# Performance work log

Measured on AMD Instinct MI355X. Metric: run time of the kernel, lower is better.

Reference implementation:

```python
import jax, jax.numpy as jnp
import numpy as np

DIM = 1024
HEADS = 16
HEAD_DIM = DIM // HEADS
NEG = -1e30
EPS = 1e-5


def _linear(x, w, b):
    # torch nn.Linear: y = x @ W^T + b, W: [out, in]
    return jnp.einsum('bnd,od->bno', x, w) + b


def _mha(x, ctx, wq, bq, wk, bk, wv, bv, wo, bo, mask):
    B, N, D = x.shape
    M = ctx.shape[1]
    q = _linear(x, wq, bq).reshape(B, N, HEADS, HEAD_DIM).transpose(0, 2, 1, 3)
    k = _linear(ctx, wk, bk).reshape(B, M, HEADS, HEAD_DIM).transpose(0, 2, 1, 3)
    v = _linear(ctx, wv, bv).reshape(B, M, HEADS, HEAD_DIM).transpose(0, 2, 1, 3)
    scores = jnp.einsum('bhqd,bhkd->bhqk', q, k) / np.sqrt(HEAD_DIM).astype(np.float32)
    if mask is not None:
        scores = jnp.where(mask == 0, NEG, scores)
    attn = jax.nn.softmax(scores, axis=-1)  # dropout = identity (eval mode)
    out = jnp.einsum('bhqk,bhkd->bhqd', attn, v)
    out = out.transpose(0, 2, 1, 3).reshape(B, N, D)
    return _linear(out, wo, bo)


def _ln(x, g, b):
    mu = jnp.mean(x, axis=-1, keepdims=True)
    var = jnp.mean(jnp.square(x - mu), axis=-1, keepdims=True)
    return (x - mu) * jax.lax.rsqrt(var + EPS) * g + b


def setup_inputs() -> dict:
    key = jax.random.key(0)
    ks = jax.random.split(key, 24)
    B, N, M = 2, 2048, 1024
    s = 0.02
    d = {
        'x': jax.random.normal(ks[0], (B, N, DIM), jnp.float32),
        'memory': jax.random.normal(ks[1], (B, M, DIM), jnp.float32),
        'mask': jnp.tril(jnp.ones((N, N), jnp.int32))[None, None],
    }
    i = 2
    for p in ['sa', 'ca']:
        for nm in ['q', 'k', 'v', 'o']:
            d[f'{p}_w{nm}'] = jax.random.normal(ks[i], (DIM, DIM), jnp.float32) * s; i += 1
            d[f'{p}_b{nm}'] = jnp.zeros((DIM,), jnp.float32)
    d['ff_w1'] = jax.random.normal(ks[i], (4 * DIM, DIM), jnp.float32) * s; i += 1
    d['ff_b1'] = jnp.zeros((4 * DIM,), jnp.float32)
    d['ff_w2'] = jax.random.normal(ks[i], (DIM, 4 * DIM), jnp.float32) * s; i += 1
    d['ff_b2'] = jnp.zeros((DIM,), jnp.float32)
    for j in (1, 2, 3):
        d[f'ln{j}_g'] = jnp.ones((DIM,), jnp.float32)
        d[f'ln{j}_b'] = jnp.zeros((DIM,), jnp.float32)
    return d


def reference(x, memory, mask,
              sa_wq, sa_bq, sa_wk, sa_bk, sa_wv, sa_bv, sa_wo, sa_bo,
              ca_wq, ca_bq, ca_wk, ca_bk, ca_wv, ca_bv, ca_wo, ca_bo,
              ff_w1, ff_b1, ff_w2, ff_b2,
              ln1_g, ln1_b, ln2_g, ln2_b, ln3_g, ln3_b):
    x = _ln(x + _mha(x, x, sa_wq, sa_bq, sa_wk, sa_bk, sa_wv, sa_bv, sa_wo, sa_bo, mask), ln1_g, ln1_b)
    x = _ln(x + _mha(x, memory, ca_wq, ca_bq, ca_wk, ca_bk, ca_wv, ca_bv, ca_wo, ca_bo, None), ln2_g, ln2_b)
    h = jax.nn.relu(_linear(x, ff_w1, ff_b1))  # dropout = identity (eval)
    x = _ln(x + _linear(h, ff_w2, ff_b2), ln3_g, ln3_b)
    return x
```

## Files before the change

kernel.cpp:

```cpp
#include <hip/hip_runtime.h>


typedef __attribute__((ext_vector_type(8))) short bf16x8;
typedef __attribute__((ext_vector_type(4))) float f32x4;

__device__ __forceinline__ unsigned short f2bf(float f) {
    union { float f; unsigned int u; } v; v.f = f;
    unsigned int r = v.u + 0x7fffu + ((v.u >> 16) & 1u);
    return (unsigned short)(r >> 16);
}
__device__ __forceinline__ float bf2f(unsigned short u) {
    union { unsigned int u; float f; } v; v.u = (unsigned int)u << 16;
    return v.f;
}
__device__ __forceinline__ unsigned int bftrunc(float f) {
    union { float f; unsigned int u; } v; v.f = f;
    return v.u >> 16;
}

struct ConvArgs {
    const float* src[12];
    unsigned short* dst[12];
    int blk_ofs[13];
    int n4[12];
    const float* bq; const float* bk; const float* bv;
    const float* ck; const float* cv;
    float* bqkv; float* bkvc;
};
__global__ __launch_bounds__(256) void conv_multi(ConvArgs a)
{
    int bid = blockIdx.x;
    if (bid >= a.blk_ofs[12]) {
        int i = (bid - a.blk_ofs[12]) * 256 + threadIdx.x;
        if (i < 1024)       a.bqkv[i] = a.bq[i];
        else if (i < 2048)  a.bqkv[i] = a.bk[i - 1024];
        else if (i < 3072)  a.bqkv[i] = a.bv[i - 2048];
        else if (i < 4096)  a.bkvc[i - 3072] = a.ck[i - 3072];
        else if (i < 5120)  a.bkvc[i - 3072] = a.cv[i - 4096];
        return;
    }
    int s = 0;
#pragma unroll
    for (int t = 0; t < 12; ++t) if (bid >= a.blk_ofs[t + 1]) s = t + 1;
    int i = (bid - a.blk_ofs[s]) * 256 + threadIdx.x;
    if (i >= a.n4[s]) return;
    float4 v = ((const float4*)a.src[s])[i];
    ushort4 o;
    o.x = f2bf(v.x); o.y = f2bf(v.y); o.z = f2bf(v.z); o.w = f2bf(v.w);
    ((ushort4*)a.dst[s])[i] = o;
}

template<int TM, int TN, int EPI, int SK>
__device__ __forceinline__ void gemm_body(
    unsigned short (*As)[64], unsigned short (*Bs)[64],
    const unsigned short* __restrict__ A, const unsigned short* __restrict__ W,
    const float* __restrict__ bias, unsigned short* __restrict__ out,
    int K, int Ncols, long slice_stride, int bid, int gx, int zslice)
{
    constexpr int AI = TM / 32;
    constexpr int BJ = TN / 32;

    const int tid  = threadIdx.x;
    const int lane = tid & 63;
    const int wave = tid >> 6;
    const int qd   = lane >> 4;
    const int l15  = lane & 15;
    const int wm   = (wave >> 1) * (TM / 2);
    const int wn   = (wave & 1) * (TN / 2);

    const int gpg = 8 * gx;
    const long m0 = (long)((bid / gpg) * 8 + (bid & 7)) * TM;
    const long n0 = (long)((bid % gpg) >> 3) * TN;

    f32x4 acc[AI][BJ] = {};

    const int srow = lane >> 3;
    const int scol = (((lane & 7) ^ srow)) * 8;
    const unsigned short* Ag = A + (m0 + wave * (8 * AI) + srow) * (long)K + scol;
    const unsigned short* Wg = W + (n0 + wave * (8 * BJ) + srow) * (long)K + scol;

    const int ksl   = K / SK;
    const int kbase = (SK > 1) ? zslice * ksl : 0;

    for (int k0 = kbase; k0 < kbase + ksl; k0 += 64) {
#pragma unroll
        for (int c = 0; c < AI; ++c)
            __builtin_amdgcn_global_load_lds(
                (const __attribute__((address_space(1))) unsigned int*)(Ag + (long)c * 8 * K + k0),
                (__attribute__((address_space(3))) unsigned int*)((char*)&As[0][0] + (wave * AI + c) * 1024),
                16, 0, 0);
#pragma unroll
        for (int c = 0; c < BJ; ++c)
            __builtin_amdgcn_global_load_lds(
                (const __attribute__((address_space(1))) unsigned int*)(Wg + (long)c * 8 * K + k0),
                (__attribute__((address_space(3))) unsigned int*)((char*)&Bs[0][0] + (wave * BJ + c) * 1024),
                16, 0, 0);
        __syncthreads();
#pragma unroll
        for (int kk = 0; kk < 64; kk += 32) {
            const int pg = ((((kk >> 3) + qd)) ^ (l15 & 7)) * 8;
            bf16x8 af[AI], bw[BJ];
#pragma unroll
            for (int i = 0; i < AI; ++i)
                af[i] = *(const bf16x8*)&As[wm + i * 16 + l15][pg];
#pragma unroll
            for (int j = 0; j < BJ; ++j)
                bw[j] = *(const bf16x8*)&Bs[wn + j * 16 + l15][pg];
#pragma unroll
            for (int i = 0; i < AI; ++i)
#pragma unroll
                for (int j = 0; j < BJ; ++j)
                    acc[i][j] = __builtin_amdgcn_mfma_f32_16x16x32_bf16(
                        af[i], bw[j], acc[i][j], 0, 0, 0);
        }
        __syncthreads();
    }

    unsigned short* op = out + ((SK > 1) ? (long)zslice * slice_stride : 0);
#pragma unroll
    for (int j = 0; j < BJ; ++j) {
        long col = n0 + wn + j * 16 + l15;
        float bv = (SK == 1 || zslice == 0) ? bias[col] : 0.f;
#pragma unroll
        for (int i = 0; i < AI; ++i) {
#pragma unroll
            for (int r = 0; r < 4; ++r) {
                long row = m0 + wm + i * 16 + qd * 4 + r;
                float v = acc[i][j][r] + bv;
                if (EPI == 1) v = (v > 0.f) ? v : 0.f;
                op[row * Ncols + col] = f2bf(v);
            }
        }
    }
}

template<int TM, int TN, int EPI, int SK>
__global__ __launch_bounds__(256) void gemm_bt(
    const unsigned short* __restrict__ A, const unsigned short* __restrict__ W,
    const float* __restrict__ bias, unsigned short* __restrict__ out,
    int K, int Ncols, long slice_stride)
{
    __shared__ unsigned short As[TM][64];
    __shared__ unsigned short Bs[TN][64];
    const int bid = blockIdx.y * gridDim.x + blockIdx.x;
    gemm_body<TM, TN, EPI, SK>(As, Bs, A, W, bias, out, K, Ncols, slice_stride,
                               bid, gridDim.x, (int)blockIdx.z);
}

template<int EPI, int SK>
__device__ __forceinline__ void gemm8_body(
    unsigned short* Ab, unsigned short* Bb,
    const unsigned short* __restrict__ A, const unsigned short* __restrict__ W,
    const float* __restrict__ bias, unsigned short* __restrict__ out,
    int K, int Ncols, long slice_stride, int mb, int nb, int zslice)
{
    const int tid  = threadIdx.x;
    const int lane = tid & 63;
    const int wave = tid >> 6;
    const int qd   = lane >> 4;
    const int l15  = lane & 15;
    const int wm   = (wave >> 2) * 128;
    const int wn   = (wave & 3) * 64;

    const long m0 = (long)mb * 256;
    const long n0 = (long)nb * 256;

    const int ksl   = K / SK;
    const int kbase = (SK > 1) ? zslice * ksl : 0;
    const int NG    = ksl / 64;

    f32x4 acc[8][4] = {};

    const int srow = tid >> 3;
    const int sgrp = ((tid & 7) ^ (srow & 7)) * 8;
    const unsigned short* Ag = A + (m0 + srow) * (long)K + kbase + sgrp;
    const unsigned short* Wg = W + (n0 + srow) * (long)K + kbase + sgrp;

    auto stA = [&](int db, int r0, int kt) {
        __builtin_amdgcn_global_load_lds(
            (const __attribute__((address_space(1))) unsigned int*)(Ag + (long)r0 * K + kt * 64),
            (__attribute__((address_space(3))) unsigned int*)(Ab + db * 16384 + r0 * 64 + wave * 512),
            16, 0, 0);
    };
    auto stB = [&](int db, int r0, int kt) {
        __builtin_amdgcn_global_load_lds(
            (const __attribute__((address_space(1))) unsigned int*)(Wg + (long)r0 * K + kt * 64),
            (__attribute__((address_space(3))) unsigned int*)(Bb + db * 16384 + r0 * 64 + wave * 512),
            16, 0, 0);
    };
    auto rdA = [&](int db, int row, int kk) -> bf16x8 {
        const int p = (((kk << 2) + qd) ^ (l15 & 7)) << 3;
        return *(const bf16x8*)(Ab + db * 16384 + row * 64 + p);
    };
    auto rdB = [&](int db, int row, int kk) -> bf16x8 {
        const int p = (((kk << 2) + qd) ^ (l15 & 7)) << 3;
        return *(const bf16x8*)(Bb + db * 16384 + row * 64 + p);
    };

#pragma unroll
    for (int h = 0; h < 4; ++h) stA(0, h * 64, 0);
#pragma unroll
    for (int h = 0; h < 4; ++h) stB(0, h * 64, 0);
    if (NG > 1) {
#pragma unroll
        for (int h = 0; h < 4; ++h) stB(1, h * 64, 1);
        stA(1, 0, 1); stA(1, 128, 1);
        asm volatile("s_waitcnt vmcnt(6)" ::: "memory");
    } else {
        asm volatile("s_waitcnt vmcnt(0)" ::: "memory");
    }
    __builtin_amdgcn_s_barrier();

    for (int g = 0; g < NG; ++g) {
        const int db = g & 1, ob = db ^ 1;
        bf16x8 af[4][2], bw[4][2];

        if (g + 1 < NG) { stA(ob, 64, g + 1); stA(ob, 192, g + 1); }

#pragma unroll
        for (int i = 0; i < 4; ++i)
#pragma unroll
            for (int kk = 0; kk < 2; ++kk)
                af[i][kk] = rdA(db, wm + i * 16 + l15, kk);
#pragma unroll
        for (int j = 0; j < 4; ++j)
#pragma unroll
            for (int kk = 0; kk < 2; ++kk)
                bw[j][kk] = rdB(db, wn + j * 16 + l15, kk);
        __builtin_amdgcn_s_setprio(1);
#pragma unroll
        for (int i = 0; i < 4; ++i)
#pragma unroll
            for (int j = 0; j < 4; ++j) {
                acc[i][j] = __builtin_amdgcn_mfma_f32_16x16x32_bf16(af[i][0], bw[j][0], acc[i][j], 0, 0, 0);
                acc[i][j] = __builtin_amdgcn_mfma_f32_16x16x32_bf16(af[i][1], bw[j][1], acc[i][j], 0, 0, 0);
            }
        __builtin_amdgcn_s_setprio(0);
        __builtin_amdgcn_s_barrier();

        if (g + 2 < NG) {
#pragma unroll
            for (int h = 0; h < 4; ++h) stB(db, h * 64, g + 2);
            stA(db, 0, g + 2); stA(db, 128, g + 2);
        }

#pragma unroll
        for (int i = 0; i < 4; ++i)
#pragma unroll
            for (int kk = 0; kk < 2; ++kk)
                af[i][kk] = rdA(db, wm + 64 + i * 16 + l15, kk);
        __builtin_amdgcn_s_setprio(1);
#pragma unroll
        for (int i = 0; i < 4; ++i)
#pragma unroll
            for (int j = 0; j < 4; ++j) {
                acc[4 + i][j] = __builtin_amdgcn_mfma_f32_16x16x32_bf16(af[i][0], bw[j][0], acc[4 + i][j], 0, 0, 0);
                acc[4 + i][j] = __builtin_amdgcn_mfma_f32_16x16x32_bf16(af[i][1], bw[j][1], acc[4 + i][j], 0, 0, 0);
            }
        __builtin_amdgcn_s_setprio(0);

        if (g + 2 < NG)      { asm volatile("s_waitcnt vmcnt(6)" ::: "memory"); }
        else if (g + 1 < NG) { asm volatile("s_waitcnt vmcnt(0)" ::: "memory"); }
        __builtin_amdgcn_s_barrier();
    }

    unsigned short* op = out + ((SK > 1) ? (long)zslice * slice_stride : 0);
#pragma unroll
    for (int j = 0; j < 4; ++j) {
        long col = n0 + wn + j * 16 + l15;
        float bv = (SK == 1 || zslice == 0) ? bias[col] : 0.f;
#pragma unroll
        for (int i = 0; i < 8; ++i) {
#pragma unroll
            for (int r = 0; r < 4; ++r) {
                long row = m0 + wm + (i >> 2) * 64 + (i & 3) * 16 + qd * 4 + r;
                float v = acc[i][j][r] + bv;
                if (EPI == 1) v = (v > 0.f) ? v : 0.f;
                op[row * Ncols + col] = f2bf(v);
            }
        }
    }
}

template<int EPI, int SK, int MODE>
__global__ __launch_bounds__(512) void gemm8_bt(
    const unsigned short* __restrict__ A, const unsigned short* __restrict__ W,
    const float* __restrict__ bias, unsigned short* __restrict__ out,
    int K, int Ncols, long slice_stride)
{
    extern __shared__ unsigned short smem[];
    const int bid = blockIdx.x;
    const int x = bid & 7;
    const int s = bid >> 3;
    int mb, nb, z = 0;
    if (MODE == 1) {
        mb = (x >> 1) * 4 + (s & 3);
        nb = (x & 1) * 8 + (s >> 2);
    } else {
        z  = x >> 1;
        mb = (x & 1) * 8 + (s & 7);
        nb = s >> 3;
    }
    gemm8_body<EPI, SK>(smem, smem + 32768, A, W, bias, out, K, Ncols,
                        slice_stride, mb, nb, z);
}

__global__ __launch_bounds__(512) void gemm8_dual(
    const unsigned short* A0, const unsigned short* W0, const float* b0,
    unsigned short* o0, int K0, int N0,
    const unsigned short* A1, const unsigned short* W1, const float* b1,
    unsigned short* o1, int K1, int N1)
{
    extern __shared__ unsigned short smem[];
    const int bid = blockIdx.x;
    const int x = bid & 7;
    const int s = bid >> 3;
    if (s < 24) {
        const int mb = (x >> 1) * 4 + (s & 3);
        const int nb = (x & 1) * 6 + (s >> 2);
        gemm8_body<0, 1>(smem, smem + 32768, A0, W0, b0, o0, K0, N0, 0, mb, nb, 0);
    } else {
        const int t = s - 24;
        const int mb = (x >> 1) * 2 + (t & 1);
        const int nb = (x & 1) * 4 + (t >> 1);
        gemm8_body<0, 1>(smem, smem + 32768, A1, W1, b1, o1, K1, N1, 0, mb, nb, 0);
    }
}

__global__ __launch_bounds__(256) void attn_kernel(
    const unsigned short* __restrict__ Qb, int q_stride,
    const unsigned short* __restrict__ KVb, int kv_stride, int koff, int voff,
    unsigned short* __restrict__ O,
    int Nq, int Mk, int causal)
{
    __shared__ unsigned short Ks[64][64];
    __shared__ unsigned short Vs[64][64];
    __shared__ unsigned short Ps[4][16][64];

    const int tid  = threadIdx.x;
    const int lane = tid & 63;
    const int wave = tid >> 6;
    const int qd   = lane >> 4;
    const int l15  = lane & 15;
    const int l7   = l15 & 7;
    const int h    = blockIdx.y;
    const int b    = blockIdx.z;
    int jq = blockIdx.x;
    if (causal && (b & 1)) jq = gridDim.x - 1 - jq;
    const int q0 = jq * 64;
    const int tb = q0 + wave * 16;

    bf16x8 aq0, aq1;
    {
        const unsigned short* qp =
            Qb + (long)(b * Nq + tb + l15) * q_stride + h * 64 + qd * 8;
        aq0 = *(const bf16x8*)qp;
        aq1 = *(const bf16x8*)(qp + 32);
    }

    float lpart[4] = {};
    f32x4 oacc[4] = {};

    const int krow  = tid >> 3;
    const int kcol  = (tid & 7) * 8;
    const int kcolS = (((tid & 7) ^ (krow & 7))) * 8;
    const int vj   = tid & 31;
    const int va_k = (vj & 15) + ((vj & 16) << 1);
    const int vfg  = (tid >> 5) * 8;
    const int vpc  = (va_k & 15) * 4 + (va_k >> 4);

    const unsigned short* Kg = KVb + (long)b * Mk * kv_stride + koff + h * 64;
    const unsigned short* Vg = KVb + (long)b * Mk * kv_stride + voff + h * 64;

    bf16x8 kr0, kr1, vra, vrb;
    auto prefetch = [&](int k0) {
        kr0 = *(const bf16x8*)(Kg + (long)(k0 + krow) * kv_stride + kcol);
        kr1 = *(const bf16x8*)(Kg + (long)(k0 + krow + 32) * kv_stride + kcol);
        const unsigned short* v0 = Vg + (long)(k0 + va_k) * kv_stride + vfg;
        vra = *(const bf16x8*)v0;
        vrb = *(const bf16x8*)(v0 + 16 * kv_stride);
    };

    const int nk = causal ? (q0 + 64) : Mk;
    prefetch(0);
    const float SCL = 0.125f * 1.44269504f;

    for (int k0 = 0; k0 < nk; k0 += 64) {
        __syncthreads();
        *(bf16x8*)&Ks[krow][kcolS]      = kr0;
        *(bf16x8*)&Ks[krow + 32][kcolS] = kr1;
#pragma unroll
        for (int jf = 0; jf < 8; ++jf) {
            unsigned int d = (unsigned short)vra[jf] |
                             ((unsigned int)(unsigned short)vrb[jf] << 16);
            const int row = vfg + jf;
            *(unsigned int*)&Vs[row][vpc ^ ((row & 7) << 3)] = d;
        }
        if (k0 + 64 < nk) prefetch(k0 + 64);
        __syncthreads();

        if (!causal || (k0 <= tb + 15)) {
            bf16x8 bk[4][2];
#pragma unroll
            for (int kt = 0; kt < 4; ++kt)
#pragma unroll
                for (int c = 0; c < 2; ++c)
                    bk[kt][c] = *(const bf16x8*)&Ks[kt * 16 + l15][((c * 4 + qd) ^ l7) * 8];
            f32x4 s[4];
#pragma unroll
            for (int kt = 0; kt < 4; ++kt) {
                f32x4 z = {};
                z = __builtin_amdgcn_mfma_f32_16x16x32_bf16(aq0, bk[kt][0], z, 0, 0, 0);
                z = __builtin_amdgcn_mfma_f32_16x16x32_bf16(aq1, bk[kt][1], z, 0, 0, 0);
                s[kt] = z;
            }
            const bool needmask = causal && (k0 + 63 > tb);
#pragma unroll
            for (int r = 0; r < 4; ++r) {
                const int qg = tb + qd * 4 + r;
                float e[4];
#pragma unroll
                for (int kt = 0; kt < 4; ++kt) {
                    float ev = __builtin_amdgcn_exp2f(s[kt][r] * SCL);
                    if (needmask && (k0 + kt * 16 + l15 > qg)) ev = 0.f;
                    e[kt] = ev;
                }
                lpart[r] += (e[0] + e[1]) + (e[2] + e[3]);
                unsigned int lo = bftrunc(e[0]) | (bftrunc(e[1]) << 16);
                unsigned int hi = bftrunc(e[2]) | (bftrunc(e[3]) << 16);
                uint2 pk; pk.x = lo; pk.y = hi;
                const int prow = qd * 4 + r;
                *(uint2*)&Ps[wave][prow][(l15 * 4) ^ ((prow & 7) << 3)] = pk;
            }
            bf16x8 bv[4][2];
#pragma unroll
            for (int dt = 0; dt < 4; ++dt)
#pragma unroll
                for (int c = 0; c < 2; ++c)
                    bv[dt][c] = *(const bf16x8*)&Vs[dt * 16 + l15][((c * 4 + qd) ^ l7) * 8];
            bf16x8 ap0 = *(const bf16x8*)&Ps[wave][l15][(qd ^ l7) * 8];
            bf16x8 ap1 = *(const bf16x8*)&Ps[wave][l15][((4 + qd) ^ l7) * 8];
#pragma unroll
            for (int dt = 0; dt < 4; ++dt) {
                oacc[dt] = __builtin_amdgcn_mfma_f32_16x16x32_bf16(
                    ap0, bv[dt][0], oacc[dt], 0, 0, 0);
                oacc[dt] = __builtin_amdgcn_mfma_f32_16x16x32_bf16(
                    ap1, bv[dt][1], oacc[dt], 0, 0, 0);
            }
        }
    }

#pragma unroll
    for (int r = 0; r < 4; ++r) {
        float l = lpart[r];
        l += __shfl_xor(l, 1);
        l += __shfl_xor(l, 2);
        l += __shfl_xor(l, 4);
        l += __shfl_xor(l, 8);
        float inv = 1.f / l;
        long row = (long)(b * Nq + tb + qd * 4 + r);
#pragma unroll
        for (int dt = 0; dt < 4; ++dt)
            O[row * 1024 + h * 64 + dt * 16 + l15] = f2bf(oacc[dt][r] * inv);
    }
}

template<int ND, int RESBF>
__global__ __launch_bounds__(256) void ln_res_kernel(
    const void* __restrict__ res, const unsigned short* __restrict__ delta,
    long dstride, const float* __restrict__ g, const float* __restrict__ beta,
    float* __restrict__ yout, unsigned short* __restrict__ ybf)
{
    __shared__ float red[8];
    const int row = blockIdx.x;
    const int tid = threadIdx.x;
    const long base = (long)row * 1024 + tid * 4;
    float v0, v1, v2, v3;
    if (RESBF) {
        ushort4 a = *(const ushort4*)((const unsigned short*)res + base);
        v0 = bf2f(a.x); v1 = bf2f(a.y); v2 = bf2f(a.z); v3 = bf2f(a.w);
    } else {
        float4 a = *(const float4*)((const float*)res + base);
        v0 = a.x; v1 = a.y; v2 = a.z; v3 = a.w;
    }
#pragma unroll
    for (int t = 0; t < ND; ++t) {
        ushort4 d = *(const ushort4*)(delta + t * dstride + base);
        v0 += bf2f(d.x); v1 += bf2f(d.y); v2 += bf2f(d.z); v3 += bf2f(d.w);
    }
    float s  = v0 + v1 + v2 + v3;
    float ss = v0 * v0 + v1 * v1 + v2 * v2 + v3 * v3;
#pragma unroll
    for (int off = 1; off < 64; off <<= 1) {
        s  += __shfl_xor(s, off);
        ss += __shfl_xor(ss, off);
    }
    const int wave = tid >> 6;
    if ((tid & 63) == 0) { red[wave] = s; red[4 + wave] = ss; }
    __syncthreads();
    float st  = red[0] + red[1] + red[2] + red[3];
    float sst = red[4] + red[5] + red[6] + red[7];
    float mean = st * (1.f / 1024.f);
    float var  = sst * (1.f / 1024.f) - mean * mean;
    float inv  = rsqrtf(var + 1e-5f);
    const int c = tid * 4;
    float y0 = (v0 - mean) * inv * g[c + 0] + beta[c + 0];
    float y1 = (v1 - mean) * inv * g[c + 1] + beta[c + 1];
    float y2 = (v2 - mean) * inv * g[c + 2] + beta[c + 2];
    float y3 = (v3 - mean) * inv * g[c + 3] + beta[c + 3];
    if (yout) *(float4*)(yout + base) = make_float4(y0, y1, y2, y3);
    if (ybf) {
        ushort4 o;
        o.x = f2bf(y0); o.y = f2bf(y1); o.z = f2bf(y2); o.w = f2bf(y3);
        *(ushort4*)(ybf + base) = o;
    }
}

extern "C" void kernel_launch(void* const* d_in, const int* in_sizes, int n_in,
                              void* d_out, int out_size, void* d_ws, size_t ws_size,
                              hipStream_t stream)
{
    const int B = 2, N = 2048, M = 1024, D = 1024, FF = 4096;
    const int TN = B * N;
    const int TM = B * M;
    const size_t MB = 1024 * 1024;

    const float* x     = (const float*)d_in[0];
    const float* mem   = (const float*)d_in[1];
    const float* sa_wq = (const float*)d_in[3];  const float* sa_bq = (const float*)d_in[4];
    const float* sa_wk = (const float*)d_in[5];  const float* sa_bk = (const float*)d_in[6];
    const float* sa_wv = (const float*)d_in[7];  const float* sa_bv = (const float*)d_in[8];
    const float* sa_wo = (const float*)d_in[9];  const float* sa_bo = (const float*)d_in[10];
    const float* ca_wq = (const float*)d_in[11]; const float* ca_bq = (const float*)d_in[12];
    const float* ca_wk = (const float*)d_in[13]; const float* ca_bk = (const float*)d_in[14];
    const float* ca_wv = (const float*)d_in[15]; const float* ca_bv = (const float*)d_in[16];
    const float* ca_wo = (const float*)d_in[17]; const float* ca_bo = (const float*)d_in[18];
    const float* ff_w1 = (const float*)d_in[19]; const float* ff_b1 = (const float*)d_in[20];
    const float* ff_w2 = (const float*)d_in[21]; const float* ff_b2 = (const float*)d_in[22];
    const float* ln1_g = (const float*)d_in[23]; const float* ln1_b = (const float*)d_in[24];
    const float* ln2_g = (const float*)d_in[25]; const float* ln2_b = (const float*)d_in[26];
    const float* ln3_g = (const float*)d_in[27]; const float* ln3_b = (const float*)d_in[28];

    char* w = (char*)d_ws;
    size_t off = 0;
    auto alloc = [&](size_t bytes) -> char* {
        char* p = w + off; off += (bytes + 255) & ~(size_t)255; return p;
    };

    unsigned short* xb   = (unsigned short*)alloc((size_t)TN * D * 2);
    unsigned short* memb = (unsigned short*)alloc((size_t)TM * D * 2);
    unsigned short* wqkv = (unsigned short*)alloc((size_t)3 * D * D * 2);
    unsigned short* wos  = (unsigned short*)alloc((size_t)D * D * 2);
    unsigned short* wqc  = (unsigned short*)alloc((size_t)D * D * 2);
    unsigned short* wkvc = (unsigned short*)alloc((size_t)2 * D * D * 2);
    unsigned short* woc  = (unsigned short*)alloc((size_t)D * D * 2);
    unsigned short* w1b  = (unsigned short*)alloc((size_t)FF * D * 2);
    unsigned short* w2b  = (unsigned short*)alloc((size_t)D * FF * 2);
    char* big = alloc((size_t)80 * MB);
    unsigned short* qkv   = (unsigned short*)big;
    unsigned short* ab    = (unsigned short*)(big + 24 * MB);
    unsigned short* kvb   = (unsigned short*)(big + 32 * MB);
    unsigned short* qb    = (unsigned short*)(big + 40 * MB);
    unsigned short* hb    = (unsigned short*)big;
    unsigned short* tmpbf = (unsigned short*)(big + 48 * MB);
    const long      TSL   = (long)TN * D;
    float* bqkv = (float*)alloc((size_t)3 * D * 4);
    float* bkvc = (float*)alloc((size_t)2 * D * 4);

    ConvArgs ca;
    const float* srcs[12] = {x, mem, sa_wq, sa_wk, sa_wv, sa_wo,
                             ca_wq, ca_wk, ca_wv, ca_wo, ff_w1, ff_w2};
    unsigned short* dsts[12] = {xb, memb, wqkv, wqkv + (size_t)D * D,
                                wqkv + (size_t)2 * D * D, wos, wqc, wkvc,
                                wkvc + (size_t)D * D, woc, w1b, w2b};
    long ns[12] = {(long)TN * D, (long)TM * D, (long)D * D, (long)D * D,
                   (long)D * D, (long)D * D, (long)D * D, (long)D * D,
                   (long)D * D, (long)D * D, (long)FF * D, (long)D * FF};
    int total_blk = 0;
    for (int i = 0; i < 12; ++i) {
        ca.src[i] = srcs[i]; ca.dst[i] = dsts[i];
        ca.n4[i] = (int)(ns[i] / 4);
        ca.blk_ofs[i] = total_blk;
        total_blk += (ca.n4[i] + 255) / 256;
    }
    ca.blk_ofs[12] = total_blk;
    ca.bq = sa_bq; ca.bk = sa_bk; ca.bv = sa_bv; ca.ck = ca_bk; ca.cv = ca_bv;
    ca.bqkv = bqkv; ca.bkvc = bkvc;
    conv_multi<<<dim3(total_blk + 20), dim3(256), 0, stream>>>(ca);

    dim3 blk(256);
    dim3 blk8(512);
    const unsigned int LDS8 = 131072;

    gemm8_dual<<<dim3(256), blk8, LDS8, stream>>>(
        xb,   wqkv, bqkv, qkv, D, 3 * D,
        memb, wkvc, bkvc, kvb, D, 2 * D);

    attn_kernel<<<dim3(N / 64, 16, B), blk, 0, stream>>>(
        qkv, 3 * D, qkv, 3 * D, D, 2 * D, ab, N, N, 1);
    gemm_bt<128, 64, 0, 2><<<dim3(D / 64, TN / 128, 2), blk, 0, stream>>>(
        ab, wos, sa_bo, tmpbf, D, D, TSL);
    ln_res_kernel<2, 0><<<dim3(TN), blk, 0, stream>>>(
        x, tmpbf, TSL, ln1_g, ln1_b, nullptr, xb);

    gemm_bt<128, 64, 0, 1><<<dim3(D / 64, TN / 128), blk, 0, stream>>>(
        xb, wqc, ca_bq, qb, D, D, 0);
    attn_kernel<<<dim3(N / 64, 16, B), blk, 0, stream>>>(
        qb, D, kvb, 2 * D, 0, D, ab, N, M, 0);
    gemm_bt<128, 64, 0, 2><<<dim3(D / 64, TN / 128, 2), blk, 0, stream>>>(
        ab, woc, ca_bo, tmpbf, D, D, TSL);
    ln_res_kernel<2, 1><<<dim3(TN), blk, 0, stream>>>(
        xb, tmpbf, TSL, ln2_g, ln2_b, nullptr, xb);

    gemm8_bt<1, 1, 1><<<dim3(256), blk8, LDS8, stream>>>(
        xb, w1b, ff_b1, hb, D, FF, 0);
    gemm8_bt<0, 4, 2><<<dim3(256), blk8, LDS8, stream>>>(
        hb, w2b, ff_b2, tmpbf, FF, D, TSL);
    ln_res_kernel<4, 1><<<dim3(TN), blk, 0, stream>>>(
        xb, tmpbf, TSL, ln3_g, ln3_b, (float*)d_out, nullptr);
}
```

Before: 455.5 us.

## Prescale Q, use byte-perm packing in attention, drop split-K in output GEMMs

Q is pre-multiplied by the softmax scale (in log2 units) on load, which removes a multiply per score in the inner loop. The V transpose and P bf16 packing now use v_perm byte shuffles. The output projections and the FF2 GEMM change from 128x64 split-K tiles, whose partial sums the LayerNorm kernel had to add up, to 128x128 tiles with no split, and FF2 moves off the 512-thread gemm8 kernel. This cuts partial-sum traffic, but it also launches fewer blocks, and rounding the scaled Q to bf16 adds a small precision change.

Result: slower. 494.7 us (+8.6%).

```diff
diff --git a/kernel.cpp b/kernel.cpp
--- a/kernel.cpp
+++ b/kernel.cpp
@@ -13,9 +13,9 @@
     union { unsigned int u; float f; } v; v.u = (unsigned int)u << 16;
     return v.f;
 }
-__device__ __forceinline__ unsigned int bftrunc(float f) {
+__device__ __forceinline__ unsigned int fbits(float f) {
     union { float f; unsigned int u; } v; v.f = f;
-    return v.u >> 16;
+    return v.u;
 }
 
 struct ConvArgs {
@@ -350,12 +350,19 @@
     const int q0 = jq * 64;
     const int tb = q0 + wave * 16;
 
+    const float SCL = 0.125f * 1.44269504f;
+
     bf16x8 aq0, aq1;
     {
         const unsigned short* qp =
             Qb + (long)(b * Nq + tb + l15) * q_stride + h * 64 + qd * 8;
         aq0 = *(const bf16x8*)qp;
         aq1 = *(const bf16x8*)(qp + 32);
+#pragma unroll
+        for (int j = 0; j < 8; ++j) {
+            aq0[j] = (short)f2bf(bf2f((unsigned short)aq0[j]) * SCL);
+            aq1[j] = (short)f2bf(bf2f((unsigned short)aq1[j]) * SCL);
+        }
     }
 
     float lpart[4] = {};
@@ -383,18 +390,22 @@
 
     const int nk = causal ? (q0 + 64) : Mk;
     prefetch(0);
-    const float SCL = 0.125f * 1.44269504f;
 
     for (int k0 = 0; k0 < nk; k0 += 64) {
         __syncthreads();
         *(bf16x8*)&Ks[krow][kcolS]      = kr0;
         *(bf16x8*)&Ks[krow + 32][kcolS] = kr1;
-#pragma unroll
-        for (int jf = 0; jf < 8; ++jf) {
-            unsigned int d = (unsigned short)vra[jf] |
-                             ((unsigned int)(unsigned short)vrb[jf] << 16);
-            const int row = vfg + jf;
-            *(unsigned int*)&Vs[row][vpc ^ ((row & 7) << 3)] = d;
+        {
+            const unsigned int* pa = (const unsigned int*)&vra;
+            const unsigned int* pb = (const unsigned int*)&vrb;
+#pragma unroll
+            for (int w2 = 0; w2 < 4; ++w2) {
+                unsigned int d0 = __builtin_amdgcn_perm(pb[w2], pa[w2], 0x05040100u);
+                unsigned int d1 = __builtin_amdgcn_perm(pb[w2], pa[w2], 0x07060302u);
+                const int r0 = vfg + 2 * w2, r1 = r0 + 1;
+                *(unsigned int*)&Vs[r0][vpc ^ ((r0 & 7) << 3)] = d0;
+                *(unsigned int*)&Vs[r1][vpc ^ ((r1 & 7) << 3)] = d1;
+            }
         }
         if (k0 + 64 < nk) prefetch(k0 + 64);
         __syncthreads();
@@ -421,13 +432,13 @@
                 float e[4];
 #pragma unroll
                 for (int kt = 0; kt < 4; ++kt) {
-                    float ev = __builtin_amdgcn_exp2f(s[kt][r] * SCL);
+                    float ev = __builtin_amdgcn_exp2f(s[kt][r]);
                     if (needmask && (k0 + kt * 16 + l15 > qg)) ev = 0.f;
                     e[kt] = ev;
                 }
                 lpart[r] += (e[0] + e[1]) + (e[2] + e[3]);
-                unsigned int lo = bftrunc(e[0]) | (bftrunc(e[1]) << 16);
-                unsigned int hi = bftrunc(e[2]) | (bftrunc(e[3]) << 16);
+                unsigned int lo = __builtin_amdgcn_perm(fbits(e[1]), fbits(e[0]), 0x07060302u);
+                unsigned int hi = __builtin_amdgcn_perm(fbits(e[3]), fbits(e[2]), 0x07060302u);
                 uint2 pk; pk.x = lo; pk.y = hi;
                 const int prow = qd * 4 + r;
                 *(uint2*)&Ps[wave][prow][(l15 * 4) ^ ((prow & 7) << 3)] = pk;
@@ -598,24 +609,24 @@
 
     attn_kernel<<<dim3(N / 64, 16, B), blk, 0, stream>>>(
         qkv, 3 * D, qkv, 3 * D, D, 2 * D, ab, N, N, 1);
-    gemm_bt<128, 64, 0, 2><<<dim3(D / 64, TN / 128, 2), blk, 0, stream>>>(
-        ab, wos, sa_bo, tmpbf, D, D, TSL);
-    ln_res_kernel<2, 0><<<dim3(TN), blk, 0, stream>>>(
+    gemm_bt<128, 128, 0, 1><<<dim3(D / 128, TN / 128), blk, 0, stream>>>(
+        ab, wos, sa_bo, tmpbf, D, D, 0);
+    ln_res_kernel<1, 0><<<dim3(TN), blk, 0, stream>>>(
         x, tmpbf, TSL, ln1_g, ln1_b, nullptr, xb);
 
-    gemm_bt<128, 64, 0, 1><<<dim3(D / 64, TN / 128), blk, 0, stream>>>(
+    gemm_bt<128, 128, 0, 1><<<dim3(D / 128, TN / 128), blk, 0, stream>>>(
         xb, wqc, ca_bq, qb, D, D, 0);
     attn_kernel<<<dim3(N / 64, 16, B), blk, 0, stream>>>(
         qb, D, kvb, 2 * D, 0, D, ab, N, M, 0);
-    gemm_bt<128, 64, 0, 2><<<dim3(D / 64, TN / 128, 2), blk, 0, stream>>>(
-        ab, woc, ca_bo, tmpbf, D, D, TSL);
-    ln_res_kernel<2, 1><<<dim3(TN), blk, 0, stream>>>(
+    gemm_bt<128, 128, 0, 1><<<dim3(D / 128, TN / 128), blk, 0, stream>>>(
+        ab, woc, ca_bo, tmpbf, D, D, 0);
+    ln_res_kernel<1, 1><<<dim3(TN), blk, 0, stream>>>(
         xb, tmpbf, TSL, ln2_g, ln2_b, nullptr, xb);
 
     gemm8_bt<1, 1, 1><<<dim3(256), blk8, LDS8, stream>>>(
         xb, w1b, ff_b1, hb, D, FF, 0);
-    gemm8_bt<0, 4, 2><<<dim3(256), blk8, LDS8, stream>>>(
-        hb, w2b, ff_b2, tmpbf, FF, D, TSL);
-    ln_res_kernel<4, 1><<<dim3(TN), blk, 0, stream>>>(
+    gemm_bt<128, 128, 0, 1><<<dim3(D / 128, TN / 128), blk, 0, stream>>>(
+        hb, w2b, ff_b2, tmpbf, FF, D, 0);
+    ln_res_kernel<1, 1><<<dim3(TN), blk, 0, stream>>>(
         xb, tmpbf, TSL, ln3_g, ln3_b, (float*)d_out, nullptr);
 }
```
